# Kernel tuning notes

Hardware: AMD Instinct MI355X
Metric: run time of the kernel (lower is better)

Reference implementation:

```python
import jax, jax.numpy as jnp
import numpy as np

B, N, C, H = 4, 1024, 1024, 16
D = C // H                      # head_dim = 64
FFH = int(int(C * 4.0) * 2 / 3) # 2730
EPS = 1e-6


def rmsnorm(x, w):
    return w * (x * jax.lax.rsqrt(jnp.mean(x * x, axis=-1, keepdims=True) + EPS))


def setup_inputs() -> dict:
    key = jax.random.key(0)
    ks = jax.random.split(key, 12)
    s = 0.02
    return {
        "x": jax.random.normal(ks[0], (B, N, C), jnp.float32),
        "c": jax.random.normal(ks[1], (B, C), jnp.float32),
        "norm1_w": jnp.ones((C,), jnp.float32),
        "norm2_w": jnp.ones((C,), jnp.float32),
        "qkv_w": jax.random.normal(ks[2], (3 * C, C), jnp.float32) * s,
        "qkv_b": jnp.zeros((3 * C,), jnp.float32),
        "q_norm_w": jnp.ones((D,), jnp.float32),
        "k_norm_w": jnp.ones((D,), jnp.float32),
        "proj_w": jax.random.normal(ks[3], (C, C), jnp.float32) * s,
        "proj_b": jnp.zeros((C,), jnp.float32),
        "w12_w": jax.random.normal(ks[4], (2 * FFH, C), jnp.float32) * s,
        "w12_b": jnp.zeros((2 * FFH,), jnp.float32),
        "w3_w": jax.random.normal(ks[5], (C, FFH), jnp.float32) * s,
        "w3_b": jnp.zeros((C,), jnp.float32),
        "ada_w": jax.random.normal(ks[6], (6 * C, C), jnp.float32) * s,
        "ada_b": jnp.zeros((6 * C,), jnp.float32),
    }


def modulate(x, shift, scale):
    return x * (1.0 + scale[:, None, :]) + shift[:, None, :]


def attention(x, qkv_w, qkv_b, q_norm_w, k_norm_w, proj_w, proj_b):
    qkv = x @ qkv_w.T + qkv_b                       # (B,N,3C)
    qkv = qkv.reshape(B, N, 3, H, D)
    q, k, v = qkv[:, :, 0], qkv[:, :, 1], qkv[:, :, 2]   # (B,N,H,D)
    q = jnp.transpose(q, (0, 2, 1, 3))              # (B,H,N,D)
    k = jnp.transpose(k, (0, 2, 1, 3))
    v = jnp.transpose(v, (0, 2, 1, 3))
    q = rmsnorm(q, q_norm_w)
    k = rmsnorm(k, k_norm_w)
    attn = jnp.einsum("bhnd,bhmd->bhnm", q, k) / jnp.sqrt(jnp.float32(D))
    attn = jax.nn.softmax(attn, axis=-1)
    out = jnp.einsum("bhnm,bhmd->bhnd", attn, v)
    out = jnp.transpose(out, (0, 2, 1, 3)).reshape(B, N, C)
    return out @ proj_w.T + proj_b


def swiglu(x, w12_w, w12_b, w3_w, w3_b):
    x12 = x @ w12_w.T + w12_b                       # (B,N,2*FFH)
    x1, x2 = x12[..., :FFH], x12[..., FFH:]
    h = jax.nn.silu(x1) * x2
    return h @ w3_w.T + w3_b


def reference(x, c, norm1_w, norm2_w, qkv_w, qkv_b, q_norm_w, k_norm_w,
              proj_w, proj_b, w12_w, w12_b, w3_w, w3_b, ada_w, ada_b):
    ada = jax.nn.silu(c) @ ada_w.T + ada_b          # (B,6C)
    s1, g1, b1, s2, g2, b2 = jnp.split(ada, 6, axis=-1)
    a = attention(modulate(rmsnorm(x, norm1_w), s1, g1),
                  qkv_w, qkv_b, q_norm_w, k_norm_w, proj_w, proj_b)
    x = x + b1[:, None, :] * a
    m = swiglu(modulate(rmsnorm(x, norm2_w), s2, g2), w12_w, w12_b, w3_w, w3_b)
    x = x + b2[:, None, :] * m
    return x
```

## Files before the change

kernel.cpp:

```cpp
#include <hip/hip_runtime.h>

typedef short s16x8 __attribute__((ext_vector_type(8)));
typedef short s16x4 __attribute__((ext_vector_type(4)));
typedef float f32x4 __attribute__((ext_vector_type(4)));

#define B_   4
#define N_   1024
#define C_   1024
#define H_   16
#define D_   64
#define FFH_ 2730
#define FFP_ 2752
#define M_   4096

__device__ __forceinline__ short f2bf(float f) {
  unsigned u = __float_as_uint(f);
  u += 0x7fff + ((u >> 16) & 1);
  return (short)(unsigned short)(u >> 16);
}
__device__ __forceinline__ float silu(float x) { return x / (1.f + __expf(-x)); }

__device__ __forceinline__ void gload16(const void* g, void* l) {
  __builtin_amdgcn_global_load_lds(
      (const __attribute__((address_space(1))) unsigned*)g,
      (__attribute__((address_space(3))) unsigned*)l, 16, 0, 0);
}

__global__ void cvt_bf(const float* __restrict__ s, short* __restrict__ d, const int n4) {
  for (int i = blockIdx.x * 256 + threadIdx.x; i < n4; i += gridDim.x * 256) {
    const float4 v = ((const float4*)s)[i];
    s16x4 o;
    o[0] = f2bf(v.x); o[1] = f2bf(v.y); o[2] = f2bf(v.z); o[3] = f2bf(v.w);
    *(s16x4*)(d + (size_t)i * 4) = o;
  }
}

__global__ void cvt_w3(const float* __restrict__ s, short* __restrict__ d) {
  const int col = blockIdx.x * 256 + threadIdx.x;
  const int row = blockIdx.y;
  if (col < FFP_)
    d[(size_t)row * FFP_ + col] = (col < FFH_) ? f2bf(s[(size_t)row * FFH_ + col]) : (short)0;
}

__global__ void ada_gemm(const float* __restrict__ c, const float* __restrict__ aw,
                         const float* __restrict__ ab, float* __restrict__ ada) {
  const int j = blockIdx.x;
  const int l = threadIdx.x;
  float acc[4] = {0.f, 0.f, 0.f, 0.f};
  const float4* wr = (const float4*)(aw + (size_t)j * 1024);
  #pragma unroll
  for (int p = 0; p < 4; ++p) {
    const float4 wv = wr[p * 64 + l];
    #pragma unroll
    for (int b = 0; b < 4; ++b) {
      const float4 cv = ((const float4*)(c + b * 1024))[p * 64 + l];
      acc[b] += silu(cv.x) * wv.x + silu(cv.y) * wv.y + silu(cv.z) * wv.z + silu(cv.w) * wv.w;
    }
  }
  #pragma unroll
  for (int b = 0; b < 4; ++b) {
    float a = acc[b];
    #pragma unroll
    for (int m = 1; m < 64; m <<= 1) a += __shfl_xor(a, m);
    if (l == 0) ada[b * 6144 + j] = a + ab[j];
  }
}

__global__ void rmsmod(const float* __restrict__ x, const float* __restrict__ wn,
                       const float* __restrict__ ada, const int sOff, const int gOff,
                       short* __restrict__ out) {
  const int row = blockIdx.x;
  const int b = row >> 10;
  const int t = threadIdx.x;
  const float4 v = ((const float4*)(x + (size_t)row * 1024))[t];
  float ss = v.x * v.x + v.y * v.y + v.z * v.z + v.w * v.w;
  #pragma unroll
  for (int m = 1; m < 64; m <<= 1) ss += __shfl_xor(ss, m);
  __shared__ float red[4];
  if ((t & 63) == 0) red[t >> 6] = ss;
  __syncthreads();
  const float rs = rsqrtf((red[0] + red[1] + red[2] + red[3]) * (1.f / 1024.f) + 1e-6f);
  const int j = t * 4;
  const float* sp = ada + b * 6144 + sOff + j;
  const float* gp = ada + b * 6144 + gOff + j;
  s16x4 o;
  o[0] = f2bf(v.x * rs * wn[j + 0] * (1.f + gp[0]) + sp[0]);
  o[1] = f2bf(v.y * rs * wn[j + 1] * (1.f + gp[1]) + sp[1]);
  o[2] = f2bf(v.z * rs * wn[j + 2] * (1.f + gp[2]) + sp[2]);
  o[3] = f2bf(v.w * rs * wn[j + 3] * (1.f + gp[3]) + sp[3]);
  *(s16x4*)(out + (size_t)row * 1024 + j) = o;
}

template <int EPI>
__launch_bounds__(256, 2)
__global__ void gemm_bt(const short* __restrict__ A, const short* __restrict__ Bt,
                        const int K, const int ldo,
                        const float* __restrict__ bias,
                        const float* __restrict__ adav,
                        const float* __restrict__ resid,
                        float* __restrict__ outF) {
  __shared__ short As[128 * 64];
  __shared__ short Bs[128 * 64];
  const int t = threadIdx.x;
  const int l = t & 63;
  const int w = t >> 6;
  const int wr = (w >> 1) * 64, wc = (w & 1) * 64;

  const int nwg = gridDim.x * gridDim.y;
  int lin = blockIdx.y * gridDim.x + blockIdx.x;
  lin = (lin & 7) * (nwg >> 3) + (lin >> 3);
  const int m0 = (lin / gridDim.x) * 128;
  const int n0 = (lin % gridDim.x) * 128;
  const int nT = K >> 6;

  f32x4 acc[4][4];
  const f32x4 z4 = {0.f, 0.f, 0.f, 0.f};
  #pragma unroll
  for (int i = 0; i < 4; ++i)
    #pragma unroll
    for (int j = 0; j < 4; ++j) acc[i][j] = z4;

  const int lr = l >> 3;
  const int lc = (l & 7) ^ lr;
  const short* gAs = A + (size_t)(m0 + w * 32 + lr) * K + lc * 8;
  const short* gBs = Bt + (size_t)(n0 + w * 32 + lr) * K + lc * 8;
  short* lA = As + (w * 32) * 64;
  short* lB = Bs + (w * 32) * 64;

  for (int kt = 0; kt < nT; ++kt) {
    if (kt) __syncthreads();
    const int ko = kt * 64;
    #pragma unroll
    for (int p = 0; p < 4; ++p) {
      gload16(gAs + (size_t)p * 8 * K + ko, lA + p * 8 * 64);
      gload16(gBs + (size_t)p * 8 * K + ko, lB + p * 8 * 64);
    }
    __syncthreads();
    #pragma unroll
    for (int kk = 0; kk < 2; ++kk) {
      const int c16 = kk * 4 + (l >> 4);
      s16x8 af[4], bfr[4];
      #pragma unroll
      for (int mf = 0; mf < 4; ++mf) {
        const int r = wr + mf * 16 + (l & 15);
        af[mf] = *(const s16x8*)&As[r * 64 + ((c16 ^ (r & 7)) << 3)];
      }
      #pragma unroll
      for (int nf = 0; nf < 4; ++nf) {
        const int r = wc + nf * 16 + (l & 15);
        bfr[nf] = *(const s16x8*)&Bs[r * 64 + ((c16 ^ (r & 7)) << 3)];
      }
      __builtin_amdgcn_s_setprio(1);
      #pragma unroll
      for (int mf = 0; mf < 4; ++mf)
        #pragma unroll
        for (int nf = 0; nf < 4; ++nf)
          acc[mf][nf] = __builtin_amdgcn_mfma_f32_16x16x32_bf16(af[mf], bfr[nf], acc[mf][nf], 0, 0, 0);
      __builtin_amdgcn_s_setprio(0);
    }
  }

  const int bIdx = m0 >> 10;
  #pragma unroll
  for (int mf = 0; mf < 4; ++mf) {
    const int row = m0 + wr + mf * 16 + ((l >> 4) << 2);
    #pragma unroll
    for (int nf = 0; nf < 4; ++nf) {
      const int col = n0 + wc + nf * 16 + (l & 15);
      const float bsv = bias[col];
      #pragma unroll
      for (int i = 0; i < 4; ++i) {
        float v = acc[mf][nf][i] + bsv;
        if (EPI == 1)
          v = resid[(size_t)(row + i) * 1024 + col] + adav[bIdx * 6144 + col] * v;
        outF[(size_t)(row + i) * ldo + col] = v;
      }
    }
  }
}

__launch_bounds__(256, 2)
__global__ void gemm_w12(const short* __restrict__ A, const short* __restrict__ Bt,
                         const float* __restrict__ bias, short* __restrict__ outH) {
  __shared__ short As[128 * 64];
  __shared__ short B1s[128 * 64];
  __shared__ short B2s[128 * 64];
  const int t = threadIdx.x;
  const int l = t & 63;
  const int w = t >> 6;
  const int wr = (w >> 1) * 64, wc = (w & 1) * 64;

  const int nwg = gridDim.x * gridDim.y;
  int lin = blockIdx.y * gridDim.x + blockIdx.x;
  lin = (lin & 7) * (nwg >> 3) + (lin >> 3);
  const int m0 = (lin / gridDim.x) * 128;
  const int n0 = (lin % gridDim.x) * 128;

  f32x4 a1[4][4], a2[4][4];
  const f32x4 z4 = {0.f, 0.f, 0.f, 0.f};
  #pragma unroll
  for (int i = 0; i < 4; ++i)
    #pragma unroll
    for (int j = 0; j < 4; ++j) { a1[i][j] = z4; a2[i][j] = z4; }

  const int lr = l >> 3;
  const int lc = (l & 7) ^ lr;
  const short* gAs = A + (size_t)(m0 + w * 32 + lr) * 1024 + lc * 8;
  const int rbase = n0 + w * 32 + lr;
  short* lA = As + (w * 32) * 64;
  short* lB1 = B1s + (w * 32) * 64;
  short* lB2 = B2s + (w * 32) * 64;

  for (int kt = 0; kt < 16; ++kt) {
    if (kt) __syncthreads();
    const int ko = kt * 64;
    #pragma unroll
    for (int p = 0; p < 4; ++p) {
      int j = rbase + p * 8;
      if (j >= FFH_) j = FFH_ - 1;
      gload16(gAs + (size_t)p * 8 * 1024 + ko, lA + p * 8 * 64);
      gload16(Bt + (size_t)j * 1024 + ko + lc * 8, lB1 + p * 8 * 64);
      gload16(Bt + (size_t)(j + FFH_) * 1024 + ko + lc * 8, lB2 + p * 8 * 64);
    }
    __syncthreads();
    #pragma unroll
    for (int kk = 0; kk < 2; ++kk) {
      const int c16 = kk * 4 + (l >> 4);
      s16x8 af[4], b1f[4], b2f[4];
      #pragma unroll
      for (int mf = 0; mf < 4; ++mf) {
        const int r = wr + mf * 16 + (l & 15);
        af[mf] = *(const s16x8*)&As[r * 64 + ((c16 ^ (r & 7)) << 3)];
      }
      #pragma unroll
      for (int nf = 0; nf < 4; ++nf) {
        const int r = wc + nf * 16 + (l & 15);
        const int idx = r * 64 + ((c16 ^ (r & 7)) << 3);
        b1f[nf] = *(const s16x8*)&B1s[idx];
        b2f[nf] = *(const s16x8*)&B2s[idx];
      }
      __builtin_amdgcn_s_setprio(1);
      #pragma unroll
      for (int mf = 0; mf < 4; ++mf)
        #pragma unroll
        for (int nf = 0; nf < 4; ++nf) {
          a1[mf][nf] = __builtin_amdgcn_mfma_f32_16x16x32_bf16(af[mf], b1f[nf], a1[mf][nf], 0, 0, 0);
          a2[mf][nf] = __builtin_amdgcn_mfma_f32_16x16x32_bf16(af[mf], b2f[nf], a2[mf][nf], 0, 0, 0);
        }
      __builtin_amdgcn_s_setprio(0);
    }
  }

  #pragma unroll
  for (int mf = 0; mf < 4; ++mf) {
    const int row = m0 + wr + mf * 16 + ((l >> 4) << 2);
    #pragma unroll
    for (int nf = 0; nf < 4; ++nf) {
      const int col = n0 + wc + nf * 16 + (l & 15);
      if (col < FFP_) {
        const bool real = col < FFH_;
        const float bb1 = real ? bias[col] : 0.f;
        const float bb2 = real ? bias[col + FFH_] : 0.f;
        #pragma unroll
        for (int i = 0; i < 4; ++i) {
          float o = 0.f;
          if (real) {
            const float v1 = a1[mf][nf][i] + bb1;
            const float v2 = a2[mf][nf][i] + bb2;
            o = silu(v1) * v2;
          }
          outH[(size_t)(row + i) * FFP_ + col] = f2bf(o);
        }
      }
    }
  }
}

__global__ void qk_post(const float* __restrict__ qkvf, const float* __restrict__ qnw,
                        const float* __restrict__ knw, short* __restrict__ qb,
                        short* __restrict__ kb) {
  const int gw = blockIdx.x * 4 + (threadIdx.x >> 6);
  const int l = threadIdx.x & 63;
  const int h = gw & 15, n = (gw >> 4) & 1023, b = gw >> 14;
  const size_t base = (size_t)(b * 1024 + n) * 3072 + h * 64 + l;
  const float qv = qkvf[base];
  const float kv = qkvf[base + 1024];
  float sq = qv * qv, sk = kv * kv;
  #pragma unroll
  for (int m = 1; m < 64; m <<= 1) { sq += __shfl_xor(sq, m); sk += __shfl_xor(sk, m); }
  const float rq = rsqrtf(sq * (1.f / 64.f) + 1e-6f);
  const float rk = rsqrtf(sk * (1.f / 64.f) + 1e-6f);
  const size_t o = ((size_t)(b * 16 + h) * 1024 + n) * 64 + l;
  qb[o] = f2bf(qv * rq * qnw[l] * 0.125f);
  kb[o] = f2bf(kv * rk * knw[l]);
}

__global__ void v_trans(const float* __restrict__ qkvf, short* __restrict__ vt) {
  __shared__ float ld[64][65];
  const int t = threadIdx.x;
  const int bh = blockIdx.y, b = bh >> 4, h = bh & 15;
  const int n0 = blockIdx.x * 64;
  const int nl = t >> 2, cb = (t & 3) * 16;
  const float* src = qkvf + (size_t)(b * 1024 + n0 + nl) * 3072 + 2048 + h * 64 + cb;
  #pragma unroll
  for (int p = 0; p < 16; ++p) ld[nl][cb + p] = src[p];
  __syncthreads();
  const int d = t >> 2, np = (t & 3) * 16;
  short* dst = vt + (size_t)(bh * 64 + d) * 1024 + n0 + np;
  #pragma unroll
  for (int p = 0; p < 16; ++p) dst[p] = f2bf(ld[np + p][d]);
}

__launch_bounds__(256, 2)
__global__ void attn(const short* __restrict__ qb, const short* __restrict__ kb,
                     const short* __restrict__ vt, short* __restrict__ ob) {
  __shared__ short Ks[64 * 64];
  __shared__ short Vs[64 * 64];
  __shared__ short Pl[4][32 * 64];
  const int t = threadIdx.x, l = t & 63, w = t >> 6;
  const int bh = blockIdx.y, b = bh >> 4, h = bh & 15;
  const int q0 = blockIdx.x * 128 + w * 32;
  const short* qp = qb + (size_t)bh * (N_ * D_);
  const short* kp = kb + (size_t)bh * (N_ * D_);
  const short* vp = vt + (size_t)bh * (D_ * N_);

  s16x8 qf[2][2];
  #pragma unroll
  for (int mf = 0; mf < 2; ++mf)
    #pragma unroll
    for (int kk = 0; kk < 2; ++kk)
      qf[mf][kk] = *(const s16x8*)&qp[(q0 + mf * 16 + (l & 15)) * 64 + kk * 32 + ((l >> 4) * 8)];

  f32x4 aco[2][4];
  float rm[2][4], rl[2][4];
  const f32x4 z4 = {0.f, 0.f, 0.f, 0.f};
  #pragma unroll
  for (int mf = 0; mf < 2; ++mf) {
    #pragma unroll
    for (int nd = 0; nd < 4; ++nd) aco[mf][nd] = z4;
    #pragma unroll
    for (int i = 0; i < 4; ++i) { rm[mf][i] = -1e30f; rl[mf][i] = 0.f; }
  }

  const int sr = t >> 2, sc = (t & 3) * 2;
  s16x8 rk[2], rv[2];
  #pragma unroll
  for (int p = 0; p < 2; ++p) {
    rk[p] = *(const s16x8*)&kp[sr * 64 + (sc + p) * 8];
    rv[p] = *(const s16x8*)&vp[sr * 1024 + (sc + p) * 8];
  }

  for (int kt = 0; kt < 16; ++kt) {
    if (kt) __syncthreads();
    #pragma unroll
    for (int p = 0; p < 2; ++p) {
      const int cs = ((sc + p) ^ (sr & 7)) << 3;
      *(s16x8*)&Ks[sr * 64 + cs] = rk[p];
      *(s16x8*)&Vs[sr * 64 + cs] = rv[p];
    }
    __syncthreads();
    if (kt < 15) {
      const int kv0 = (kt + 1) * 64;
      #pragma unroll
      for (int p = 0; p < 2; ++p) {
        rk[p] = *(const s16x8*)&kp[(kv0 + sr) * 64 + (sc + p) * 8];
        rv[p] = *(const s16x8*)&vp[sr * 1024 + kv0 + (sc + p) * 8];
      }
    }

    f32x4 s[2][4];
    #pragma unroll
    for (int mf = 0; mf < 2; ++mf)
      #pragma unroll
      for (int nf = 0; nf < 4; ++nf) s[mf][nf] = z4;

    #pragma unroll
    for (int kk = 0; kk < 2; ++kk) {
      const int c16 = kk * 4 + (l >> 4);
      s16x8 kf[4];
      #pragma unroll
      for (int nf = 0; nf < 4; ++nf) {
        const int r = nf * 16 + (l & 15);
        kf[nf] = *(const s16x8*)&Ks[r * 64 + ((c16 ^ (r & 7)) << 3)];
      }
      __builtin_amdgcn_s_setprio(1);
      #pragma unroll
      for (int mf = 0; mf < 2; ++mf)
        #pragma unroll
        for (int nf = 0; nf < 4; ++nf)
          s[mf][nf] = __builtin_amdgcn_mfma_f32_16x16x32_bf16(qf[mf][kk], kf[nf], s[mf][nf], 0, 0, 0);
      __builtin_amdgcn_s_setprio(0);
    }

    #pragma unroll
    for (int mf = 0; mf < 2; ++mf) {
      #pragma unroll
      for (int i = 0; i < 4; ++i) {
        float pm = fmaxf(fmaxf(s[mf][0][i], s[mf][1][i]), fmaxf(s[mf][2][i], s[mf][3][i]));
        pm = fmaxf(pm, __shfl_xor(pm, 1));
        pm = fmaxf(pm, __shfl_xor(pm, 2));
        pm = fmaxf(pm, __shfl_xor(pm, 4));
        pm = fmaxf(pm, __shfl_xor(pm, 8));
        const float nm = fmaxf(rm[mf][i], pm);
        const float corr = __expf(rm[mf][i] - nm);
        rm[mf][i] = nm;
        float rs = 0.f;
        #pragma unroll
        for (int nf = 0; nf < 4; ++nf) {
          const float p = __expf(s[mf][nf][i] - nm);
          s[mf][nf][i] = p;
          rs += p;
        }
        rs += __shfl_xor(rs, 1);
        rs += __shfl_xor(rs, 2);
        rs += __shfl_xor(rs, 4);
        rs += __shfl_xor(rs, 8);
        rl[mf][i] = rl[mf][i] * corr + rs;
        #pragma unroll
        for (int nd = 0; nd < 4; ++nd) aco[mf][nd][i] *= corr;
      }
    }

    short* pw = &Pl[w][0];
    #pragma unroll
    for (int mf = 0; mf < 2; ++mf)
      #pragma unroll
      for (int nf = 0; nf < 4; ++nf)
        #pragma unroll
        for (int i = 0; i < 4; ++i) {
          const int row = mf * 16 + ((l >> 4) << 2) + i;
          const int col = nf * 16 + (l & 15);
          pw[row * 64 + (((col >> 3) ^ (row & 7)) << 3) + (col & 7)] = f2bf(s[mf][nf][i]);
        }

    #pragma unroll
    for (int kk = 0; kk < 2; ++kk) {
      const int c16 = kk * 4 + (l >> 4);
      s16x8 vf[4];
      #pragma unroll
      for (int nd = 0; nd < 4; ++nd) {
        const int r = nd * 16 + (l & 15);
        vf[nd] = *(const s16x8*)&Vs[r * 64 + ((c16 ^ (r & 7)) << 3)];
      }
      __builtin_amdgcn_s_setprio(1);
      #pragma unroll
      for (int mf = 0; mf < 2; ++mf) {
        const int pr = mf * 16 + (l & 15);
        const s16x8 pf = *(const s16x8*)&pw[pr * 64 + ((c16 ^ (pr & 7)) << 3)];
        #pragma unroll
        for (int nd = 0; nd < 4; ++nd)
          aco[mf][nd] = __builtin_amdgcn_mfma_f32_16x16x32_bf16(pf, vf[nd], aco[mf][nd], 0, 0, 0);
      }
      __builtin_amdgcn_s_setprio(0);
    }
  }

  #pragma unroll
  for (int mf = 0; mf < 2; ++mf)
    #pragma unroll
    for (int i = 0; i < 4; ++i) {
      const float inv = 1.f / rl[mf][i];
      const int row = q0 + mf * 16 + ((l >> 4) << 2) + i;
      #pragma unroll
      for (int nd = 0; nd < 4; ++nd) {
        const int col = h * 64 + nd * 16 + (l & 15);
        ob[(size_t)(b * 1024 + row) * 1024 + col] = f2bf(aco[mf][nd][i] * inv);
      }
    }
}

extern "C" void kernel_launch(void* const* d_in, const int* in_sizes, int n_in,
                              void* d_out, int out_size, void* d_ws, size_t ws_size,
                              hipStream_t stream) {
  const float* x     = (const float*)d_in[0];
  const float* c     = (const float*)d_in[1];
  const float* n1w   = (const float*)d_in[2];
  const float* n2w   = (const float*)d_in[3];
  const float* qkvw  = (const float*)d_in[4];
  const float* qkvb  = (const float*)d_in[5];
  const float* qnw   = (const float*)d_in[6];
  const float* knw   = (const float*)d_in[7];
  const float* projw = (const float*)d_in[8];
  const float* projb = (const float*)d_in[9];
  const float* w12w  = (const float*)d_in[10];
  const float* w12b  = (const float*)d_in[11];
  const float* w3w   = (const float*)d_in[12];
  const float* w3b   = (const float*)d_in[13];
  const float* adaw  = (const float*)d_in[14];
  const float* adab  = (const float*)d_in[15];
  float* outp = (float*)d_out;

  char* ws = (char*)d_ws;
  size_t off = 0;
  auto alloc = [&](size_t bytes) { void* p = ws + off; off += (bytes + 255) & ~(size_t)255; return p; };
  short* WQKV = (short*)alloc(3072ull * 1024 * 2);
  short* WPROJ = (short*)alloc(1024ull * 1024 * 2);
  short* W12B = (short*)alloc(5460ull * 1024 * 2);
  short* W3B = (short*)alloc(1024ull * 2752 * 2);
  float* ADA = (float*)alloc(4ull * 6144 * 4);
  short* H1 = (short*)alloc(4096ull * 1024 * 2);
  float* QKVF = (float*)alloc(4096ull * 3072 * 4);
  short* QBF = (short*)alloc(64ull * 1024 * 64 * 2);
  short* KBF = (short*)alloc(64ull * 1024 * 64 * 2);
  short* VTB = (short*)alloc(64ull * 64 * 1024 * 2);
  short* OBF = (short*)alloc(4096ull * 1024 * 2);
  float* X1 = (float*)alloc(4096ull * 1024 * 4);
  short* H2 = (short*)alloc(4096ull * 1024 * 2);
  short* HB = (short*)alloc(4096ull * 2752 * 2);

  cvt_bf<<<2048, 256, 0, stream>>>(qkvw, WQKV, 3072 * 1024 / 4);
  cvt_bf<<<1024, 256, 0, stream>>>(projw, WPROJ, 1024 * 1024 / 4);
  cvt_bf<<<2048, 256, 0, stream>>>(w12w, W12B, 5460 * 1024 / 4);
  cvt_w3<<<dim3(11, 1024), 256, 0, stream>>>(w3w, W3B);
  ada_gemm<<<6144, 64, 0, stream>>>(c, adaw, adab, ADA);
  rmsmod<<<4096, 256, 0, stream>>>(x, n1w, ADA, 0, 1024, H1);
  gemm_bt<0><<<dim3(24, 32), 256, 0, stream>>>(H1, WQKV, 1024, 3072, qkvb, nullptr, nullptr, QKVF);
  qk_post<<<16384, 256, 0, stream>>>(QKVF, qnw, knw, QBF, KBF);
  v_trans<<<dim3(16, 64), 256, 0, stream>>>(QKVF, VTB);
  attn<<<dim3(8, 64), 256, 0, stream>>>(QBF, KBF, VTB, OBF);
  gemm_bt<1><<<dim3(8, 32), 256, 0, stream>>>(OBF, WPROJ, 1024, 1024, projb, ADA + 2048, x, X1);
  rmsmod<<<4096, 256, 0, stream>>>(X1, n2w, ADA, 3072, 4096, H2);
  gemm_w12<<<dim3(22, 32), 256, 0, stream>>>(H2, W12B, w12b, HB);
  gemm_bt<1><<<dim3(8, 32), 256, 0, stream>>>(HB, W3B, 2752, 1024, w3b, ADA + 5120, X1, outp);
}
```

Measured before the change: 295.4 us.

## Double-buffer GEMM tiles, fuse QK-norm and SwiGLU epilogues, interleave w12 weights

Merges the GEMM kernels into one templated kernel that double-buffers the LDS A/B tiles, so each k-step prefetches the next tile and needs one barrier instead of two. The QKV GEMM epilogue now applies the per-head q/k RMSNorm and writes bf16 Q/K directly, and writes V as bf16 rows. This removes the fp32 QKV intermediate and the separate qk_post kernel, and makes the V transpose work on bf16. The w12 weights are pre-interleaved so x1/x2 pairs sit in adjacent columns, letting the SwiGLU run as a lane-shuffle epilogue on a plain GEMM. In exchange, LDS use doubles, and the padding columns of the SwiGLU output are no longer explicitly zeroed.

```diff
diff --git a/kernel.cpp b/kernel.cpp
--- a/kernel.cpp
+++ b/kernel.cpp
@@ -11,7 +11,7 @@
 #define D_   64
 #define FFH_ 2730
 #define FFP_ 2752
-#define M_   4096
+#define FFI_ 5632
 
 __device__ __forceinline__ short f2bf(float f) {
   unsigned u = __float_as_uint(f);
@@ -40,6 +40,20 @@
   const int row = blockIdx.y;
   if (col < FFP_)
     d[(size_t)row * FFP_ + col] = (col < FFH_) ? f2bf(s[(size_t)row * FFH_ + col]) : (short)0;
+}
+
+__global__ void cvt_w12i(const float* __restrict__ s, short* __restrict__ d) {
+  const int r = blockIdx.y;
+  const int cb = threadIdx.x * 4;
+  s16x4 o;
+  if (r < 2 * FFH_) {
+    const int j = (r >> 1) + (r & 1) * FFH_;
+    const float4 v = *(const float4*)(s + (size_t)j * 1024 + cb);
+    o[0] = f2bf(v.x); o[1] = f2bf(v.y); o[2] = f2bf(v.z); o[3] = f2bf(v.w);
+  } else {
+    o[0] = 0; o[1] = 0; o[2] = 0; o[3] = 0;
+  }
+  *(s16x4*)(d + (size_t)r * 1024 + cb) = o;
 }
 
 __global__ void ada_gemm(const float* __restrict__ c, const float* __restrict__ aw,
@@ -93,14 +107,18 @@
 
 template <int EPI>
 __launch_bounds__(256, 2)
-__global__ void gemm_bt(const short* __restrict__ A, const short* __restrict__ Bt,
-                        const int K, const int ldo,
+__global__ void gemm2ph(const short* __restrict__ A, const short* __restrict__ Bt,
+                        const int K,
                         const float* __restrict__ bias,
                         const float* __restrict__ adav,
                         const float* __restrict__ resid,
-                        float* __restrict__ outF) {
-  __shared__ short As[128 * 64];
-  __shared__ short Bs[128 * 64];
+                        float* __restrict__ outF,
+                        short* __restrict__ outB,
+                        short* __restrict__ qbO, short* __restrict__ kbO,
+                        short* __restrict__ vrO,
+                        const float* __restrict__ qnw, const float* __restrict__ knw) {
+  __shared__ short As[2][128 * 64];
+  __shared__ short Bs[2][128 * 64];
   const int t = threadIdx.x;
   const int l = t & 63;
   const int w = t >> 6;
@@ -124,18 +142,23 @@
   const int lc = (l & 7) ^ lr;
   const short* gAs = A + (size_t)(m0 + w * 32 + lr) * K + lc * 8;
   const short* gBs = Bt + (size_t)(n0 + w * 32 + lr) * K + lc * 8;
-  short* lA = As + (w * 32) * 64;
-  short* lB = Bs + (w * 32) * 64;
+  const int wofs = w * 32 * 64;
+
+#define STAGE_(buf, kt)                                                        \
+  do {                                                                         \
+    const int _ko = (kt) * 64;                                                 \
+    _Pragma("unroll") for (int p = 0; p < 4; ++p) {                            \
+      gload16(gAs + (size_t)p * 8 * K + _ko, &As[buf][wofs + p * 8 * 64]);     \
+      gload16(gBs + (size_t)p * 8 * K + _ko, &Bs[buf][wofs + p * 8 * 64]);     \
+    }                                                                          \
+  } while (0)
+
+  STAGE_(0, 0);
+  __syncthreads();
 
   for (int kt = 0; kt < nT; ++kt) {
-    if (kt) __syncthreads();
-    const int ko = kt * 64;
-    #pragma unroll
-    for (int p = 0; p < 4; ++p) {
-      gload16(gAs + (size_t)p * 8 * K + ko, lA + p * 8 * 64);
-      gload16(gBs + (size_t)p * 8 * K + ko, lB + p * 8 * 64);
-    }
-    __syncthreads();
+    const int cur = kt & 1;
+    if (kt + 1 < nT) STAGE_(cur ^ 1, kt + 1);
     #pragma unroll
     for (int kk = 0; kk < 2; ++kk) {
       const int c16 = kk * 4 + (l >> 4);
@@ -143,12 +166,12 @@
       #pragma unroll
       for (int mf = 0; mf < 4; ++mf) {
         const int r = wr + mf * 16 + (l & 15);
-        af[mf] = *(const s16x8*)&As[r * 64 + ((c16 ^ (r & 7)) << 3)];
+        af[mf] = *(const s16x8*)&As[cur][r * 64 + ((c16 ^ (r & 7)) << 3)];
       }
       #pragma unroll
       for (int nf = 0; nf < 4; ++nf) {
         const int r = wc + nf * 16 + (l & 15);
-        bfr[nf] = *(const s16x8*)&Bs[r * 64 + ((c16 ^ (r & 7)) << 3)];
+        bfr[nf] = *(const s16x8*)&Bs[cur][r * 64 + ((c16 ^ (r & 7)) << 3)];
       }
       __builtin_amdgcn_s_setprio(1);
       #pragma unroll
@@ -158,157 +181,119 @@
           acc[mf][nf] = __builtin_amdgcn_mfma_f32_16x16x32_bf16(af[mf], bfr[nf], acc[mf][nf], 0, 0, 0);
       __builtin_amdgcn_s_setprio(0);
     }
-  }
-
-  const int bIdx = m0 >> 10;
-  #pragma unroll
-  for (int mf = 0; mf < 4; ++mf) {
-    const int row = m0 + wr + mf * 16 + ((l >> 4) << 2);
-    #pragma unroll
-    for (int nf = 0; nf < 4; ++nf) {
-      const int col = n0 + wc + nf * 16 + (l & 15);
-      const float bsv = bias[col];
-      #pragma unroll
-      for (int i = 0; i < 4; ++i) {
-        float v = acc[mf][nf][i] + bsv;
-        if (EPI == 1)
-          v = resid[(size_t)(row + i) * 1024 + col] + adav[bIdx * 6144 + col] * v;
-        outF[(size_t)(row + i) * ldo + col] = v;
-      }
-    }
-  }
-}
-
-__launch_bounds__(256, 2)
-__global__ void gemm_w12(const short* __restrict__ A, const short* __restrict__ Bt,
-                         const float* __restrict__ bias, short* __restrict__ outH) {
-  __shared__ short As[128 * 64];
-  __shared__ short B1s[128 * 64];
-  __shared__ short B2s[128 * 64];
-  const int t = threadIdx.x;
-  const int l = t & 63;
-  const int w = t >> 6;
-  const int wr = (w >> 1) * 64, wc = (w & 1) * 64;
-
-  const int nwg = gridDim.x * gridDim.y;
-  int lin = blockIdx.y * gridDim.x + blockIdx.x;
-  lin = (lin & 7) * (nwg >> 3) + (lin >> 3);
-  const int m0 = (lin / gridDim.x) * 128;
-  const int n0 = (lin % gridDim.x) * 128;
-
-  f32x4 a1[4][4], a2[4][4];
-  const f32x4 z4 = {0.f, 0.f, 0.f, 0.f};
-  #pragma unroll
-  for (int i = 0; i < 4; ++i)
-    #pragma unroll
-    for (int j = 0; j < 4; ++j) { a1[i][j] = z4; a2[i][j] = z4; }
-
-  const int lr = l >> 3;
-  const int lc = (l & 7) ^ lr;
-  const short* gAs = A + (size_t)(m0 + w * 32 + lr) * 1024 + lc * 8;
-  const int rbase = n0 + w * 32 + lr;
-  short* lA = As + (w * 32) * 64;
-  short* lB1 = B1s + (w * 32) * 64;
-  short* lB2 = B2s + (w * 32) * 64;
-
-  for (int kt = 0; kt < 16; ++kt) {
-    if (kt) __syncthreads();
-    const int ko = kt * 64;
-    #pragma unroll
-    for (int p = 0; p < 4; ++p) {
-      int j = rbase + p * 8;
-      if (j >= FFH_) j = FFH_ - 1;
-      gload16(gAs + (size_t)p * 8 * 1024 + ko, lA + p * 8 * 64);
-      gload16(Bt + (size_t)j * 1024 + ko + lc * 8, lB1 + p * 8 * 64);
-      gload16(Bt + (size_t)(j + FFH_) * 1024 + ko + lc * 8, lB2 + p * 8 * 64);
-    }
     __syncthreads();
-    #pragma unroll
-    for (int kk = 0; kk < 2; ++kk) {
-      const int c16 = kk * 4 + (l >> 4);
-      s16x8 af[4], b1f[4], b2f[4];
+  }
+#undef STAGE_
+
+  if (EPI == 1) {
+    const int bIdx = m0 >> 10;
+    #pragma unroll
+    for (int mf = 0; mf < 4; ++mf) {
+      const int row = m0 + wr + mf * 16 + ((l >> 4) << 2);
+      #pragma unroll
+      for (int nf = 0; nf < 4; ++nf) {
+        const int col = n0 + wc + nf * 16 + (l & 15);
+        const float bsv = bias[col];
+        const float av = adav[bIdx * 6144 + col];
+        #pragma unroll
+        for (int i = 0; i < 4; ++i) {
+          const float v = acc[mf][nf][i] + bsv;
+          outF[(size_t)(row + i) * 1024 + col] =
+              resid[(size_t)(row + i) * 1024 + col] + av * v;
+        }
+      }
+    }
+  }
+
+  if (EPI == 2) {
+    const int colB = n0 + wc;
+    const int sec = colB >> 10;
+    const int hh = (colB >> 6) & 15;
+    if (sec < 2) {
+      short* dst = sec ? kbO : qbO;
+      const float* nw = sec ? knw : qnw;
+      const float scl = sec ? 1.f : 0.125f;
       #pragma unroll
       for (int mf = 0; mf < 4; ++mf) {
-        const int r = wr + mf * 16 + (l & 15);
-        af[mf] = *(const s16x8*)&As[r * 64 + ((c16 ^ (r & 7)) << 3)];
-      }
+        #pragma unroll
+        for (int i = 0; i < 4; ++i) {
+          const int row = m0 + wr + mf * 16 + ((l >> 4) << 2) + i;
+          float vv[4];
+          float ss = 0.f;
+          #pragma unroll
+          for (int nf = 0; nf < 4; ++nf) {
+            vv[nf] = acc[mf][nf][i] + bias[colB + nf * 16 + (l & 15)];
+            ss += vv[nf] * vv[nf];
+          }
+          ss += __shfl_xor(ss, 1); ss += __shfl_xor(ss, 2);
+          ss += __shfl_xor(ss, 4); ss += __shfl_xor(ss, 8);
+          const float rs = rsqrtf(ss * (1.f / 64.f) + 1e-6f) * scl;
+          const int bb = row >> 10, nn = row & 1023;
+          #pragma unroll
+          for (int nf = 0; nf < 4; ++nf) {
+            const int d = nf * 16 + (l & 15);
+            dst[((size_t)(bb * 16 + hh) * 1024 + nn) * 64 + d] = f2bf(vv[nf] * rs * nw[d]);
+          }
+        }
+      }
+    } else {
+      #pragma unroll
+      for (int mf = 0; mf < 4; ++mf)
+        #pragma unroll
+        for (int nf = 0; nf < 4; ++nf) {
+          const int col = colB + nf * 16 + (l & 15);
+          const float bsv = bias[col];
+          #pragma unroll
+          for (int i = 0; i < 4; ++i) {
+            const int row = m0 + wr + mf * 16 + ((l >> 4) << 2) + i;
+            vrO[(size_t)row * 1024 + (col - 2048)] = f2bf(acc[mf][nf][i] + bsv);
+          }
+        }
+    }
+  }
+
+  if (EPI == 3) {
+    #pragma unroll
+    for (int mf = 0; mf < 4; ++mf) {
       #pragma unroll
       for (int nf = 0; nf < 4; ++nf) {
-        const int r = wc + nf * 16 + (l & 15);
-        const int idx = r * 64 + ((c16 ^ (r & 7)) << 3);
-        b1f[nf] = *(const s16x8*)&B1s[idx];
-        b2f[nf] = *(const s16x8*)&B2s[idx];
-      }
-      __builtin_amdgcn_s_setprio(1);
-      #pragma unroll
-      for (int mf = 0; mf < 4; ++mf)
-        #pragma unroll
-        for (int nf = 0; nf < 4; ++nf) {
-          a1[mf][nf] = __builtin_amdgcn_mfma_f32_16x16x32_bf16(af[mf], b1f[nf], a1[mf][nf], 0, 0, 0);
-          a2[mf][nf] = __builtin_amdgcn_mfma_f32_16x16x32_bf16(af[mf], b2f[nf], a2[mf][nf], 0, 0, 0);
+        const int gc = n0 + wc + nf * 16 + (l & 15);
+        const int pc = gc >> 1;
+        const bool real = pc < FFH_;
+        const float b1 = real ? bias[pc] : 0.f;
+        const float b2 = real ? bias[FFH_ + pc] : 0.f;
+        #pragma unroll
+        for (int i = 0; i < 4; ++i) {
+          const float v = acc[mf][nf][i];
+          const float prt = __shfl_xor(v, 1);
+          if (!(l & 1) && real) {
+            const float x1 = v + b1, x2 = prt + b2;
+            const int row = m0 + wr + mf * 16 + ((l >> 4) << 2) + i;
+            outB[(size_t)row * FFP_ + pc] = f2bf(silu(x1) * x2);
+          }
         }
-      __builtin_amdgcn_s_setprio(0);
-    }
-  }
-
-  #pragma unroll
-  for (int mf = 0; mf < 4; ++mf) {
-    const int row = m0 + wr + mf * 16 + ((l >> 4) << 2);
-    #pragma unroll
-    for (int nf = 0; nf < 4; ++nf) {
-      const int col = n0 + wc + nf * 16 + (l & 15);
-      if (col < FFP_) {
-        const bool real = col < FFH_;
-        const float bb1 = real ? bias[col] : 0.f;
-        const float bb2 = real ? bias[col + FFH_] : 0.f;
-        #pragma unroll
-        for (int i = 0; i < 4; ++i) {
-          float o = 0.f;
-          if (real) {
-            const float v1 = a1[mf][nf][i] + bb1;
-            const float v2 = a2[mf][nf][i] + bb2;
-            o = silu(v1) * v2;
-          }
-          outH[(size_t)(row + i) * FFP_ + col] = f2bf(o);
-        }
-      }
-    }
-  }
-}
-
-__global__ void qk_post(const float* __restrict__ qkvf, const float* __restrict__ qnw,
-                        const float* __restrict__ knw, short* __restrict__ qb,
-                        short* __restrict__ kb) {
-  const int gw = blockIdx.x * 4 + (threadIdx.x >> 6);
-  const int l = threadIdx.x & 63;
-  const int h = gw & 15, n = (gw >> 4) & 1023, b = gw >> 14;
-  const size_t base = (size_t)(b * 1024 + n) * 3072 + h * 64 + l;
-  const float qv = qkvf[base];
-  const float kv = qkvf[base + 1024];
-  float sq = qv * qv, sk = kv * kv;
-  #pragma unroll
-  for (int m = 1; m < 64; m <<= 1) { sq += __shfl_xor(sq, m); sk += __shfl_xor(sk, m); }
-  const float rq = rsqrtf(sq * (1.f / 64.f) + 1e-6f);
-  const float rk = rsqrtf(sk * (1.f / 64.f) + 1e-6f);
-  const size_t o = ((size_t)(b * 16 + h) * 1024 + n) * 64 + l;
-  qb[o] = f2bf(qv * rq * qnw[l] * 0.125f);
-  kb[o] = f2bf(kv * rk * knw[l]);
-}
-
-__global__ void v_trans(const float* __restrict__ qkvf, short* __restrict__ vt) {
-  __shared__ float ld[64][65];
+      }
+    }
+  }
+}
+
+__global__ void v_trans(const short* __restrict__ vr, short* __restrict__ vt) {
+  __shared__ short ld[64][72];
   const int t = threadIdx.x;
   const int bh = blockIdx.y, b = bh >> 4, h = bh & 15;
   const int n0 = blockIdx.x * 64;
   const int nl = t >> 2, cb = (t & 3) * 16;
-  const float* src = qkvf + (size_t)(b * 1024 + n0 + nl) * 3072 + 2048 + h * 64 + cb;
-  #pragma unroll
-  for (int p = 0; p < 16; ++p) ld[nl][cb + p] = src[p];
+  const short* src = vr + (size_t)(b * 1024 + n0 + nl) * 1024 + h * 64 + cb;
+  *(s16x8*)&ld[nl][cb] = *(const s16x8*)src;
+  *(s16x8*)&ld[nl][cb + 8] = *(const s16x8*)(src + 8);
   __syncthreads();
   const int d = t >> 2, np = (t & 3) * 16;
   short* dst = vt + (size_t)(bh * 64 + d) * 1024 + n0 + np;
-  #pragma unroll
-  for (int p = 0; p < 16; ++p) dst[p] = f2bf(ld[np + p][d]);
+  s16x8 o0, o1;
+  #pragma unroll
+  for (int p = 0; p < 8; ++p) { o0[p] = ld[np + p][d]; o1[p] = ld[np + 8 + p][d]; }
+  *(s16x8*)dst = o0;
+  *(s16x8*)(dst + 8) = o1;
 }
 
 __launch_bounds__(256, 2)
@@ -495,31 +480,34 @@
   auto alloc = [&](size_t bytes) { void* p = ws + off; off += (bytes + 255) & ~(size_t)255; return p; };
   short* WQKV = (short*)alloc(3072ull * 1024 * 2);
   short* WPROJ = (short*)alloc(1024ull * 1024 * 2);
-  short* W12B = (short*)alloc(5460ull * 1024 * 2);
-  short* W3B = (short*)alloc(1024ull * 2752 * 2);
-  float* ADA = (float*)alloc(4ull * 6144 * 4);
-  short* H1 = (short*)alloc(4096ull * 1024 * 2);
-  float* QKVF = (float*)alloc(4096ull * 3072 * 4);
-  short* QBF = (short*)alloc(64ull * 1024 * 64 * 2);
-  short* KBF = (short*)alloc(64ull * 1024 * 64 * 2);
-  short* VTB = (short*)alloc(64ull * 64 * 1024 * 2);
-  short* OBF = (short*)alloc(4096ull * 1024 * 2);
-  float* X1 = (float*)alloc(4096ull * 1024 * 4);
-  short* H2 = (short*)alloc(4096ull * 1024 * 2);
-  short* HB = (short*)alloc(4096ull * 2752 * 2);
+  short* W12I = (short*)alloc((size_t)FFI_ * 1024 * 2);
+  short* W3B  = (short*)alloc(1024ull * FFP_ * 2);
+  float* ADA  = (float*)alloc(4ull * 6144 * 4);
+  short* H1   = (short*)alloc(4096ull * 1024 * 2);
+  short* QBF  = (short*)alloc(64ull * 1024 * 64 * 2);
+  short* KBF  = (short*)alloc(64ull * 1024 * 64 * 2);
+  short* VROW = (short*)alloc(4096ull * 1024 * 2);
+  short* VTB  = (short*)alloc(64ull * 64 * 1024 * 2);
+  short* OBF  = (short*)alloc(4096ull * 1024 * 2);
+  float* X1   = (float*)alloc(4096ull * 1024 * 4);
+  short* H2   = (short*)alloc(4096ull * 1024 * 2);
+  short* HB   = (short*)alloc(4096ull * FFP_ * 2);
 
   cvt_bf<<<2048, 256, 0, stream>>>(qkvw, WQKV, 3072 * 1024 / 4);
   cvt_bf<<<1024, 256, 0, stream>>>(projw, WPROJ, 1024 * 1024 / 4);
-  cvt_bf<<<2048, 256, 0, stream>>>(w12w, W12B, 5460 * 1024 / 4);
+  cvt_w12i<<<dim3(1, FFI_), 256, 0, stream>>>(w12w, W12I);
   cvt_w3<<<dim3(11, 1024), 256, 0, stream>>>(w3w, W3B);
   ada_gemm<<<6144, 64, 0, stream>>>(c, adaw, adab, ADA);
   rmsmod<<<4096, 256, 0, stream>>>(x, n1w, ADA, 0, 1024, H1);
-  gemm_bt<0><<<dim3(24, 32), 256, 0, stream>>>(H1, WQKV, 1024, 3072, qkvb, nullptr, nullptr, QKVF);
-  qk_post<<<16384, 256, 0, stream>>>(QKVF, qnw, knw, QBF, KBF);
-  v_trans<<<dim3(16, 64), 256, 0, stream>>>(QKVF, VTB);
+  gemm2ph<2><<<dim3(24, 32), 256, 0, stream>>>(H1, WQKV, 1024, qkvb,
+      nullptr, nullptr, nullptr, nullptr, QBF, KBF, VROW, qnw, knw);
+  v_trans<<<dim3(16, 64), 256, 0, stream>>>(VROW, VTB);
   attn<<<dim3(8, 64), 256, 0, stream>>>(QBF, KBF, VTB, OBF);
-  gemm_bt<1><<<dim3(8, 32), 256, 0, stream>>>(OBF, WPROJ, 1024, 1024, projb, ADA + 2048, x, X1);
+  gemm2ph<1><<<dim3(8, 32), 256, 0, stream>>>(OBF, WPROJ, 1024, projb,
+      ADA + 2048, x, X1, nullptr, nullptr, nullptr, nullptr, nullptr, nullptr);
   rmsmod<<<4096, 256, 0, stream>>>(X1, n2w, ADA, 3072, 4096, H2);
-  gemm_w12<<<dim3(22, 32), 256, 0, stream>>>(H2, W12B, w12b, HB);
-  gemm_bt<1><<<dim3(8, 32), 256, 0, stream>>>(HB, W3B, 2752, 1024, w3b, ADA + 5120, X1, outp);
-}
+  gemm2ph<3><<<dim3(FFI_ / 128, 32), 256, 0, stream>>>(H2, W12I, 1024, w12b,
+      nullptr, nullptr, nullptr, HB, nullptr, nullptr, nullptr, nullptr, nullptr);
+  gemm2ph<1><<<dim3(8, 32), 256, 0, stream>>>(HB, W3B, FFP_, w3b,
+      ADA + 5120, X1, outp, nullptr, nullptr, nullptr, nullptr, nullptr, nullptr);
+}
```

Result: slower. 315.5 us (+6.8%).

## Fuse q/k RMSNorm and head relayout into QKV GEMM epilogue, emit bf16 V

Applied to the files above, without the earlier changes.

The QKV GEMM epilogue now applies bias, per-head RMSNorm (reducing across the 16 lanes that hold one head row) and the q scaling, then writes bf16 Q and K directly in head-major layout. V is written as bf16 rows and transposed by a slimmer bf16 v_trans with vector loads and stores. This removes the fp32 QKV intermediate (about 50 MB written and read back) and the separate qk_post kernel. The cost is scattered 2-byte stores with poor coalescing in the epilogue.

```diff
diff --git a/kernel.cpp b/kernel.cpp
--- a/kernel.cpp
+++ b/kernel.cpp
@@ -11,7 +11,6 @@
 #define D_   64
 #define FFH_ 2730
 #define FFP_ 2752
-#define M_   4096
 
 __device__ __forceinline__ short f2bf(float f) {
   unsigned u = __float_as_uint(f);
@@ -94,11 +93,14 @@
 template <int EPI>
 __launch_bounds__(256, 2)
 __global__ void gemm_bt(const short* __restrict__ A, const short* __restrict__ Bt,
-                        const int K, const int ldo,
+                        const int K,
                         const float* __restrict__ bias,
                         const float* __restrict__ adav,
                         const float* __restrict__ resid,
-                        float* __restrict__ outF) {
+                        float* __restrict__ outF,
+                        short* __restrict__ qbO, short* __restrict__ kbO,
+                        short* __restrict__ vrO,
+                        const float* __restrict__ qnw, const float* __restrict__ knw) {
   __shared__ short As[128 * 64];
   __shared__ short Bs[128 * 64];
   const int t = threadIdx.x;
@@ -160,21 +162,70 @@
     }
   }
 
-  const int bIdx = m0 >> 10;
-  #pragma unroll
-  for (int mf = 0; mf < 4; ++mf) {
-    const int row = m0 + wr + mf * 16 + ((l >> 4) << 2);
-    #pragma unroll
-    for (int nf = 0; nf < 4; ++nf) {
-      const int col = n0 + wc + nf * 16 + (l & 15);
-      const float bsv = bias[col];
-      #pragma unroll
-      for (int i = 0; i < 4; ++i) {
-        float v = acc[mf][nf][i] + bsv;
-        if (EPI == 1)
-          v = resid[(size_t)(row + i) * 1024 + col] + adav[bIdx * 6144 + col] * v;
-        outF[(size_t)(row + i) * ldo + col] = v;
-      }
+  if (EPI == 1) {
+    const int bIdx = m0 >> 10;
+    #pragma unroll
+    for (int mf = 0; mf < 4; ++mf) {
+      const int row = m0 + wr + mf * 16 + ((l >> 4) << 2);
+      #pragma unroll
+      for (int nf = 0; nf < 4; ++nf) {
+        const int col = n0 + wc + nf * 16 + (l & 15);
+        const float bsv = bias[col];
+        const float av = adav[bIdx * 6144 + col];
+        #pragma unroll
+        for (int i = 0; i < 4; ++i) {
+          const float v = acc[mf][nf][i] + bsv;
+          outF[(size_t)(row + i) * 1024 + col] =
+              resid[(size_t)(row + i) * 1024 + col] + av * v;
+        }
+      }
+    }
+  }
+
+  if (EPI == 2) {
+    const int colB = n0 + wc;
+    const int sec = colB >> 10;
+    const int hh = (colB >> 6) & 15;
+    if (sec < 2) {
+      short* dst = sec ? kbO : qbO;
+      const float* nw = sec ? knw : qnw;
+      const float scl = sec ? 1.f : 0.125f;
+      #pragma unroll
+      for (int mf = 0; mf < 4; ++mf) {
+        #pragma unroll
+        for (int i = 0; i < 4; ++i) {
+          const int row = m0 + wr + mf * 16 + ((l >> 4) << 2) + i;
+          float vv[4];
+          float ss = 0.f;
+          #pragma unroll
+          for (int nf = 0; nf < 4; ++nf) {
+            vv[nf] = acc[mf][nf][i] + bias[colB + nf * 16 + (l & 15)];
+            ss += vv[nf] * vv[nf];
+          }
+          ss += __shfl_xor(ss, 1); ss += __shfl_xor(ss, 2);
+          ss += __shfl_xor(ss, 4); ss += __shfl_xor(ss, 8);
+          const float rs = rsqrtf(ss * (1.f / 64.f) + 1e-6f) * scl;
+          const int bb = row >> 10, nn = row & 1023;
+          #pragma unroll
+          for (int nf = 0; nf < 4; ++nf) {
+            const int d = nf * 16 + (l & 15);
+            dst[((size_t)(bb * 16 + hh) * 1024 + nn) * 64 + d] = f2bf(vv[nf] * rs * nw[d]);
+          }
+        }
+      }
+    } else {
+      #pragma unroll
+      for (int mf = 0; mf < 4; ++mf)
+        #pragma unroll
+        for (int nf = 0; nf < 4; ++nf) {
+          const int col = colB + nf * 16 + (l & 15);
+          const float bsv = bias[col];
+          #pragma unroll
+          for (int i = 0; i < 4; ++i) {
+            const int row = m0 + wr + mf * 16 + ((l >> 4) << 2) + i;
+            vrO[(size_t)row * 1024 + (col - 2048)] = f2bf(acc[mf][nf][i] + bsv);
+          }
+        }
     }
   }
 }
@@ -276,39 +327,23 @@
   }
 }
 
-__global__ void qk_post(const float* __restrict__ qkvf, const float* __restrict__ qnw,
-                        const float* __restrict__ knw, short* __restrict__ qb,
-                        short* __restrict__ kb) {
-  const int gw = blockIdx.x * 4 + (threadIdx.x >> 6);
-  const int l = threadIdx.x & 63;
-  const int h = gw & 15, n = (gw >> 4) & 1023, b = gw >> 14;
-  const size_t base = (size_t)(b * 1024 + n) * 3072 + h * 64 + l;
-  const float qv = qkvf[base];
-  const float kv = qkvf[base + 1024];
-  float sq = qv * qv, sk = kv * kv;
-  #pragma unroll
-  for (int m = 1; m < 64; m <<= 1) { sq += __shfl_xor(sq, m); sk += __shfl_xor(sk, m); }
-  const float rq = rsqrtf(sq * (1.f / 64.f) + 1e-6f);
-  const float rk = rsqrtf(sk * (1.f / 64.f) + 1e-6f);
-  const size_t o = ((size_t)(b * 16 + h) * 1024 + n) * 64 + l;
-  qb[o] = f2bf(qv * rq * qnw[l] * 0.125f);
-  kb[o] = f2bf(kv * rk * knw[l]);
-}
-
-__global__ void v_trans(const float* __restrict__ qkvf, short* __restrict__ vt) {
-  __shared__ float ld[64][65];
+__global__ void v_trans(const short* __restrict__ vr, short* __restrict__ vt) {
+  __shared__ short ld[64][72];
   const int t = threadIdx.x;
   const int bh = blockIdx.y, b = bh >> 4, h = bh & 15;
   const int n0 = blockIdx.x * 64;
   const int nl = t >> 2, cb = (t & 3) * 16;
-  const float* src = qkvf + (size_t)(b * 1024 + n0 + nl) * 3072 + 2048 + h * 64 + cb;
-  #pragma unroll
-  for (int p = 0; p < 16; ++p) ld[nl][cb + p] = src[p];
+  const short* src = vr + (size_t)(b * 1024 + n0 + nl) * 1024 + h * 64 + cb;
+  *(s16x8*)&ld[nl][cb] = *(const s16x8*)src;
+  *(s16x8*)&ld[nl][cb + 8] = *(const s16x8*)(src + 8);
   __syncthreads();
   const int d = t >> 2, np = (t & 3) * 16;
   short* dst = vt + (size_t)(bh * 64 + d) * 1024 + n0 + np;
-  #pragma unroll
-  for (int p = 0; p < 16; ++p) dst[p] = f2bf(ld[np + p][d]);
+  s16x8 o0, o1;
+  #pragma unroll
+  for (int p = 0; p < 8; ++p) { o0[p] = ld[np + p][d]; o1[p] = ld[np + 8 + p][d]; }
+  *(s16x8*)dst = o0;
+  *(s16x8*)(dst + 8) = o1;
 }
 
 __launch_bounds__(256, 2)
@@ -496,17 +531,17 @@
   short* WQKV = (short*)alloc(3072ull * 1024 * 2);
   short* WPROJ = (short*)alloc(1024ull * 1024 * 2);
   short* W12B = (short*)alloc(5460ull * 1024 * 2);
-  short* W3B = (short*)alloc(1024ull * 2752 * 2);
-  float* ADA = (float*)alloc(4ull * 6144 * 4);
-  short* H1 = (short*)alloc(4096ull * 1024 * 2);
-  float* QKVF = (float*)alloc(4096ull * 3072 * 4);
-  short* QBF = (short*)alloc(64ull * 1024 * 64 * 2);
-  short* KBF = (short*)alloc(64ull * 1024 * 64 * 2);
-  short* VTB = (short*)alloc(64ull * 64 * 1024 * 2);
-  short* OBF = (short*)alloc(4096ull * 1024 * 2);
-  float* X1 = (float*)alloc(4096ull * 1024 * 4);
-  short* H2 = (short*)alloc(4096ull * 1024 * 2);
-  short* HB = (short*)alloc(4096ull * 2752 * 2);
+  short* W3B  = (short*)alloc(1024ull * FFP_ * 2);
+  float* ADA  = (float*)alloc(4ull * 6144 * 4);
+  short* H1   = (short*)alloc(4096ull * 1024 * 2);
+  short* QBF  = (short*)alloc(64ull * 1024 * 64 * 2);
+  short* KBF  = (short*)alloc(64ull * 1024 * 64 * 2);
+  short* VROW = (short*)alloc(4096ull * 1024 * 2);
+  short* VTB  = (short*)alloc(64ull * 64 * 1024 * 2);
+  short* OBF  = (short*)alloc(4096ull * 1024 * 2);
+  float* X1   = (float*)alloc(4096ull * 1024 * 4);
+  short* H2   = (short*)alloc(4096ull * 1024 * 2);
+  short* HB   = (short*)alloc(4096ull * FFP_ * 2);
 
   cvt_bf<<<2048, 256, 0, stream>>>(qkvw, WQKV, 3072 * 1024 / 4);
   cvt_bf<<<1024, 256, 0, stream>>>(projw, WPROJ, 1024 * 1024 / 4);
@@ -514,12 +549,14 @@
   cvt_w3<<<dim3(11, 1024), 256, 0, stream>>>(w3w, W3B);
   ada_gemm<<<6144, 64, 0, stream>>>(c, adaw, adab, ADA);
   rmsmod<<<4096, 256, 0, stream>>>(x, n1w, ADA, 0, 1024, H1);
-  gemm_bt<0><<<dim3(24, 32), 256, 0, stream>>>(H1, WQKV, 1024, 3072, qkvb, nullptr, nullptr, QKVF);
-  qk_post<<<16384, 256, 0, stream>>>(QKVF, qnw, knw, QBF, KBF);
-  v_trans<<<dim3(16, 64), 256, 0, stream>>>(QKVF, VTB);
+  gemm_bt<2><<<dim3(24, 32), 256, 0, stream>>>(H1, WQKV, 1024, qkvb,
+      nullptr, nullptr, nullptr, QBF, KBF, VROW, qnw, knw);
+  v_trans<<<dim3(16, 64), 256, 0, stream>>>(VROW, VTB);
   attn<<<dim3(8, 64), 256, 0, stream>>>(QBF, KBF, VTB, OBF);
-  gemm_bt<1><<<dim3(8, 32), 256, 0, stream>>>(OBF, WPROJ, 1024, 1024, projb, ADA + 2048, x, X1);
+  gemm_bt<1><<<dim3(8, 32), 256, 0, stream>>>(OBF, WPROJ, 1024, projb,
+      ADA + 2048, x, X1, nullptr, nullptr, nullptr, nullptr, nullptr);
   rmsmod<<<4096, 256, 0, stream>>>(X1, n2w, ADA, 3072, 4096, H2);
   gemm_w12<<<dim3(22, 32), 256, 0, stream>>>(H2, W12B, w12b, HB);
-  gemm_bt<1><<<dim3(8, 32), 256, 0, stream>>>(HB, W3B, 2752, 1024, w3b, ADA + 5120, X1, outp);
-}
+  gemm_bt<1><<<dim3(8, 32), 256, 0, stream>>>(HB, W3B, FFP_, w3b,
+      ADA + 5120, X1, outp, nullptr, nullptr, nullptr, nullptr, nullptr);
+}
```

New measurement: 278.8 us. -5.6%, faster.
